# Kernel optimization log

Measured on AMD Instinct MI355X. Metric: run time of the kernel, lower is better.

Reference implementation:

```python
import jax, jax.numpy as jnp
import numpy as np

B, T, D, H, KH, HD, F, L, V = 2, 2048, 1024, 16, 4, 64, 4096, 4, 32000
G = H // KH  # num_key_value_groups
EPS = 1e-6
SCALE = HD ** -0.5


def setup_inputs() -> dict:
    key = jax.random.key(0)
    ks = jax.random.split(key, 8)
    std = 0.02
    return {
        "input_ids": jax.random.randint(ks[0], (B, T), 0, V, dtype=jnp.int32),
        "embed_w": jax.random.normal(ks[1], (V, D), jnp.float32) * std,
        "pos_w": jax.random.normal(ks[2], (T, D), jnp.float32) * std,
        "ln1_w": jnp.ones((L, D), jnp.float32),
        "ln2_w": jnp.ones((L, D), jnp.float32),
        "wq": jax.random.normal(ks[3], (L, D, H * HD), jnp.float32) * std,
        "wkv": jax.random.normal(ks[4], (L, D, 2 * KH * HD), jnp.float32) * std,
        "wo": jax.random.normal(ks[5], (L, H * HD, D), jnp.float32) * std,
        "w1": jax.random.normal(ks[6], (L, D, F), jnp.float32) * std,
        "w2": jax.random.normal(ks[7], (L, F, D), jnp.float32) * std,
        "norm_w": jnp.ones((D,), jnp.float32),
    }


def _rmsnorm(x, w):
    return x * jax.lax.rsqrt(jnp.mean(x * x, axis=-1, keepdims=True) + EPS) * w


def reference(input_ids, embed_w, pos_w, ln1_w, ln2_w, wq, wkv, wo, w1, w2, norm_w):
    causal = jnp.tril(jnp.ones((T, T), dtype=bool))  # True = keep
    x = embed_w[input_ids] + pos_w[:T]  # [B,T,D]
    for l in range(L):
        h = _rmsnorm(x, ln1_w[l])
        q = (h @ wq[l]).reshape(B, T, H, HD)
        kv = h @ wkv[l]
        k, v = jnp.split(kv, 2, axis=-1)
        k = jnp.repeat(k.reshape(B, T, KH, HD), G, axis=2)  # GQA repeat_interleave
        v = jnp.repeat(v.reshape(B, T, KH, HD), G, axis=2)
        scores = jnp.einsum("bqhd,bkhd->bhqk", q, k) * SCALE
        scores = jnp.where(causal, scores, -jnp.inf)
        p = jax.nn.softmax(scores, axis=-1)
        o = jnp.einsum("bhqk,bkhd->bqhd", p, v).reshape(B, T, H * HD)
        x = x + o @ wo[l]
        h = _rmsnorm(x, ln2_w[l])
        x = x + jax.nn.gelu(h @ w1[l], approximate=False) @ w2[l]
    x = _rmsnorm(x, norm_w)
    logits = x @ embed_w.T  # tied lm_head
    return logits
```

## Files before the change

### kernel.cpp

```cpp
#include <hip/hip_runtime.h>
#include <hip/hip_bf16.h>

#define DI __device__ __forceinline__

typedef unsigned short u16;
typedef unsigned int u32;
typedef __attribute__((ext_vector_type(8))) short bf16x8;
typedef __attribute__((ext_vector_type(4))) short bf16x4;
typedef __attribute__((ext_vector_type(4))) float f32x4;

#define B_   2
#define T_   2048
#define D_   1024
#define H_   16
#define KH_  4
#define HD_  64
#define F_   4096
#define L_   4
#define V_   32000
#define M_   (B_ * T_)
#define QKVN (H_*HD_ + 2*KH_*HD_)

DI u16 f2bf(float f) {
  __hip_bfloat16 h = __float2bfloat16(f);
  return *reinterpret_cast<u16*>(&h);
}

DI float bf2f(u16 b) {
  __hip_bfloat16 h = *reinterpret_cast<__hip_bfloat16*>(&b);
  return __bfloat162float(h);
}

DI void gl_lds16(const void* g, void* l) {
  __builtin_amdgcn_global_load_lds(
      (const __attribute__((address_space(1))) u32*)g,
      (__attribute__((address_space(3))) u32*)l, 16, 0, 0);
}

#define BARRIER() do { asm volatile("" ::: "memory"); __builtin_amdgcn_s_barrier(); asm volatile("" ::: "memory"); } while (0)
#define LGK0()    asm volatile("s_waitcnt lgkmcnt(0)" ::: "memory")
#define VMC(n)    asm volatile("s_waitcnt vmcnt(" #n ")" ::: "memory")
#define PRIO(p)   __builtin_amdgcn_s_setprio(p)

__global__ __launch_bounds__(256) void embed_kernel(const int* __restrict__ ids,
                                                    const float* __restrict__ ew,
                                                    const float* __restrict__ pw,
                                                    float* __restrict__ x) {
  const int row = blockIdx.x;
  const int t = row & (T_ - 1);
  const int id = ids[row];
  float4 e = reinterpret_cast<const float4*>(ew + (size_t)id * D_)[threadIdx.x];
  float4 p = reinterpret_cast<const float4*>(pw + (size_t)t * D_)[threadIdx.x];
  e.x += p.x; e.y += p.y; e.z += p.z; e.w += p.w;
  reinterpret_cast<float4*>(x + (size_t)row * D_)[threadIdx.x] = e;
}

__global__ __launch_bounds__(256) void conv_kernel(const float* __restrict__ W,
                                                   u16* __restrict__ Wb) {
  const size_t i = (size_t)blockIdx.x * 256 + threadIdx.x;
  float4 v = reinterpret_cast<const float4*>(W)[i];
  ushort4 ov;
  ov.x = f2bf(v.x); ov.y = f2bf(v.y); ov.z = f2bf(v.z); ov.w = f2bf(v.w);
  reinterpret_cast<ushort4*>(Wb)[i] = ov;
}

__global__ __launch_bounds__(256) void convt_fused(const float* __restrict__ wq,
                                                   const float* __restrict__ wkv,
                                                   const float* __restrict__ wo,
                                                   const float* __restrict__ w1,
                                                   const float* __restrict__ w2,
                                                   u16* __restrict__ wtq,
                                                   u16* __restrict__ wto,
                                                   u16* __restrict__ wt1,
                                                   u16* __restrict__ wt2) {
  const int t = blockIdx.x;
  const float* W; u16* Wt; int K, N, local;
  if (t < 1024)      { W = wq;  Wt = wtq;               K = 1024; N = 1024; local = t; }
  else if (t < 1536) { W = wkv; Wt = wtq + 1024*1024;   K = 1024; N = 512;  local = t - 1024; }
  else if (t < 2560) { W = wo;  Wt = wto;               K = 1024; N = 1024; local = t - 1536; }
  else if (t < 6656) { W = w1;  Wt = wt1;               K = 1024; N = 4096; local = t - 2560; }
  else               { W = w2;  Wt = wt2;               K = 4096; N = 1024; local = t - 6656; }
  const int nk = K >> 5;
  const int k0 = (local % nk) * 32, n0 = (local / nk) * 32;
  __shared__ float tb[32][33];
  const int tx = threadIdx.x & 31, ty = threadIdx.x >> 5;
  #pragma unroll
  for (int i = 0; i < 4; i++)
    tb[ty + i*8][tx] = W[(size_t)(k0 + ty + i*8) * N + n0 + tx];
  __syncthreads();
  #pragma unroll
  for (int i = 0; i < 4; i++)
    Wt[(size_t)(n0 + ty + i*8) * K + k0 + tx] = f2bf(tb[tx][ty + i*8]);
}

__global__ __launch_bounds__(256) void rmsnorm_kernel(const float* __restrict__ x,
                                                      const float* __restrict__ w,
                                                      u16* __restrict__ out) {
  const int row = blockIdx.x;
  const int tid = threadIdx.x;
  float4 v = reinterpret_cast<const float4*>(x + (size_t)row * D_)[tid];
  float ss = v.x*v.x + v.y*v.y + v.z*v.z + v.w*v.w;
  #pragma unroll
  for (int off = 32; off > 0; off >>= 1) ss += __shfl_down(ss, off, 64);
  __shared__ float red[4];
  if ((tid & 63) == 0) red[tid >> 6] = ss;
  __syncthreads();
  const float tot = red[0] + red[1] + red[2] + red[3];
  const float rstd = rsqrtf(tot * (1.0f / D_) + 1e-6f);
  float4 wv = reinterpret_cast<const float4*>(w)[tid];
  ushort4 ov;
  ov.x = f2bf(v.x * rstd * wv.x);
  ov.y = f2bf(v.y * rstd * wv.y);
  ov.z = f2bf(v.z * rstd * wv.z);
  ov.w = f2bf(v.w * rstd * wv.w);
  reinterpret_cast<ushort4*>(out + (size_t)row * D_)[tid] = ov;
}

template <int EPI>
__global__ __launch_bounds__(256) void gemm_bt(const u16* __restrict__ A,
                                               const u16* __restrict__ Bt,
                                               const float* __restrict__ res,
                                               u16* __restrict__ Cb,
                                               float* __restrict__ Cf,
                                               int M, int N, int K) {
  __shared__ u16 As[128 * 64];
  __shared__ u16 Bs[128 * 64];
  const int tid = threadIdx.x;
  const int n0 = blockIdx.x * 128;
  const int m0 = blockIdx.y * 128;
  const int lane = tid & 63, wave = tid >> 6;
  const int wm = wave >> 1, wn = wave & 1;
  const int l15 = lane & 15, l4 = lane >> 4;
  const int srow = tid >> 3, scol = (tid & 7) * 8;
  const u16* ag = A + (size_t)(m0 + srow) * K + scol;
  const u16* bg = Bt + (size_t)(n0 + srow) * K + scol;
  u16* asd = &As[srow * 64 + scol];
  u16* bsd = &Bs[srow * 64 + scol];
  f32x4 acc[4][4] = {};
  const int nk = K >> 6;
  for (int kt = 0; kt < nk; kt++) {
    const int k0 = kt * 64;
    __syncthreads();
    #pragma unroll
    for (int i = 0; i < 4; i++) gl_lds16(ag + (size_t)i*32*K + k0, asd + i*32*64);
    #pragma unroll
    for (int i = 0; i < 4; i++) gl_lds16(bg + (size_t)i*32*K + k0, bsd + i*32*64);
    __syncthreads();
    #pragma unroll
    for (int s = 0; s < 2; s++) {
      bf16x8 af[4], bfv[4];
      #pragma unroll
      for (int i = 0; i < 4; i++)
        af[i] = *reinterpret_cast<const bf16x8*>(&As[(wm*64 + i*16 + l15)*64 + s*32 + l4*8]);
      #pragma unroll
      for (int j = 0; j < 4; j++)
        bfv[j] = *reinterpret_cast<const bf16x8*>(&Bs[(wn*64 + j*16 + l15)*64 + s*32 + l4*8]);
      #pragma unroll
      for (int i = 0; i < 4; i++)
        #pragma unroll
        for (int j = 0; j < 4; j++)
          acc[i][j] = __builtin_amdgcn_mfma_f32_16x16x32_bf16(bfv[j], af[i], acc[i][j], 0, 0, 0);
    }
  }
  #pragma unroll
  for (int i = 0; i < 4; i++) {
    const int row = m0 + wm*64 + i*16 + l15;
    #pragma unroll
    for (int j = 0; j < 4; j++) {
      const int colb = n0 + wn*64 + j*16 + l4*4;
      const size_t idx = (size_t)row * N + colb;
      const f32x4 v = acc[i][j];
      if (EPI == 0) {
        ushort4 ov;
        ov.x = f2bf(v[0]); ov.y = f2bf(v[1]); ov.z = f2bf(v[2]); ov.w = f2bf(v[3]);
        *reinterpret_cast<ushort4*>(&Cb[idx]) = ov;
      } else {
        const float4 rv = *reinterpret_cast<const float4*>(&res[idx]);
        float4 ov;
        ov.x = v[0] + rv.x; ov.y = v[1] + rv.y; ov.z = v[2] + rv.z; ov.w = v[3] + rv.w;
        *reinterpret_cast<float4*>(&Cf[idx]) = ov;
      }
    }
  }
}

template <int EPI>
__global__ __launch_bounds__(512, 2) void gemm256(const u16* __restrict__ A,
                                                  const u16* __restrict__ Bt,
                                                  u16* __restrict__ Cb,
                                                  float* __restrict__ Cf,
                                                  int M, int N, int K) {
  __shared__ char lds[131072];
  char* const AsB = lds;
  char* const BsB = lds + 65536;
  const int tid = threadIdx.x;
  const int lane = tid & 63, wave = tid >> 6;
  const int wm = wave >> 2, wn = wave & 3;
  const int l15 = lane & 15, l4 = lane >> 4;

  const int nm = M >> 8;
  const int nwg = nm * (N >> 8);
  const int cpx = nwg >> 3;
  const int bid = blockIdx.x;
  const int wg = (bid & 7) * cpx + (bid >> 3);
  const int m0 = (wg % nm) << 8;
  const int n0 = (wg / nm) << 8;

  const u16* const Atile = A + (size_t)m0 * K;
  const u16* const Btile = Bt + (size_t)n0 * K;

  int soff[2][2], pd[2][2];
  #pragma unroll
  for (int h = 0; h < 2; ++h)
    #pragma unroll
    for (int jj = 0; jj < 2; ++jj) {
      const int row = h*128 + jj*64 + (tid >> 3);
      const int sl  = (tid & 7) ^ (row & 7);
      soff[h][jj] = row * K + sl * 8;
      pd[h][jj]   = h*16384 + jj*8192 + tid*16;
    }
  const int swz = (l15 & 7) << 4;
  const int rb0 = l15*128 + ((l4*16)      ^ swz);
  const int rb1 = l15*128 + ((64 + l4*16) ^ swz);

  #define STA(S,H,T) do { const u16* g_ = Atile + (T)*64; char* d_ = AsB + (S)*32768; \
      gl_lds16(g_ + soff[H][0], d_ + pd[H][0]); gl_lds16(g_ + soff[H][1], d_ + pd[H][1]); } while (0)
  #define STB(S,H,T) do { const u16* g_ = Btile + (T)*64; char* d_ = BsB + (S)*32768; \
      gl_lds16(g_ + soff[H][0], d_ + pd[H][0]); gl_lds16(g_ + soff[H][1], d_ + pd[H][1]); } while (0)
  #define RDA(S,GI,RB) (*reinterpret_cast<const bf16x8*>(AsB + (S)*32768 + (GI)*2048 + (RB)))
  #define RDB(S,GJ,RB) (*reinterpret_cast<const bf16x8*>(BsB + (S)*32768 + (GJ)*2048 + (RB)))

  f32x4 acc[8][4] = {};
  bf16x8 Ar[4][2], Br[4][2];

  #define RDA03(S) { _Pragma("unroll") for (int i=0;i<4;++i){ Ar[i][0]=RDA(S,i*2+wm,rb0); Ar[i][1]=RDA(S,i*2+wm,rb1);} }
  #define RDA47(S) { _Pragma("unroll") for (int i=0;i<4;++i){ Ar[i][0]=RDA(S,(i+4)*2+wm,rb0); Ar[i][1]=RDA(S,(i+4)*2+wm,rb1);} }
  #define RDB01(S) { _Pragma("unroll") for (int j=0;j<2;++j){ Br[j][0]=RDB(S,j*4+wn,rb0); Br[j][1]=RDB(S,j*4+wn,rb1);} }
  #define RDB23(S) { _Pragma("unroll") for (int j=2;j<4;++j){ Br[j][0]=RDB(S,j*4+wn,rb0); Br[j][1]=RDB(S,j*4+wn,rb1);} }
  #define MFQ(IO,JL) { _Pragma("unroll") for (int i=0;i<4;++i) _Pragma("unroll") for (int jj=0;jj<2;++jj) { \
      acc[(IO)+i][(JL)+jj] = __builtin_amdgcn_mfma_f32_16x16x32_bf16(Br[(JL)+jj][0], Ar[i][0], acc[(IO)+i][(JL)+jj],0,0,0); \
      acc[(IO)+i][(JL)+jj] = __builtin_amdgcn_mfma_f32_16x16x32_bf16(Br[(JL)+jj][1], Ar[i][1], acc[(IO)+i][(JL)+jj],0,0,0); } }

  STA(0,0,0); STA(0,1,0); STB(0,0,0); STB(0,1,0);
  VMC(4);
  STA(1,0,1); STB(1,0,1); STB(1,1,1);
  VMC(6);
  BARRIER();

  const int niter = K >> 7;
  for (int it = 0; it < niter; ++it) {
    const int t0 = it*2, t1 = t0 + 1;
    const bool pf = (it + 1 < niter);
    RDA03(0); RDB01(0); STA(1,1,t1);
    BARRIER(); LGK0(); PRIO(1); MFQ(0,0); PRIO(0); BARRIER();
    RDB23(0); if (pf) STA(0,0,t0+2);
    BARRIER(); LGK0(); PRIO(1); MFQ(0,2); PRIO(0); BARRIER();
    RDA47(0); if (pf) STB(0,0,t0+2);
    BARRIER(); LGK0(); PRIO(1); MFQ(4,0); PRIO(0); BARRIER();
    if (pf) { STB(0,1,t0+2); VMC(6); } else { VMC(0); }
    BARRIER(); PRIO(1); MFQ(4,2); PRIO(0); BARRIER();
    RDA03(1); RDB01(1); if (pf) STA(0,1,t0+2);
    BARRIER(); LGK0(); PRIO(1); MFQ(0,0); PRIO(0); BARRIER();
    RDB23(1); if (pf) STA(1,0,t1+2);
    BARRIER(); LGK0(); PRIO(1); MFQ(0,2); PRIO(0); BARRIER();
    RDA47(1); if (pf) STB(1,0,t1+2);
    BARRIER(); LGK0(); PRIO(1); MFQ(4,0); PRIO(0); BARRIER();
    if (pf) { STB(1,1,t1+2); VMC(6); }
    BARRIER(); PRIO(1); MFQ(4,2); PRIO(0); BARRIER();
  }

  #pragma unroll
  for (int i = 0; i < 8; ++i) {
    const int row = m0 + (i*2 + wm)*16 + l15;
    #pragma unroll
    for (int j = 0; j < 4; ++j) {
      const int colb = n0 + (j*4 + wn)*16 + l4*4;
      const f32x4 v = acc[i][j];
      if (EPI == 0) {
        *reinterpret_cast<f32x4*>(&Cf[(size_t)row * N + colb]) = v;
      } else {
        ushort4 ov;
        #pragma unroll
        for (int rr = 0; rr < 4; ++rr) {
          const float g = 0.5f * v[rr] * (1.0f + erff(v[rr] * 0.70710678118f));
          ((u16*)&ov)[rr] = f2bf(g);
        }
        *reinterpret_cast<ushort4*>(&Cb[(size_t)row * N + colb]) = ov;
      }
    }
  }
  #undef STA
  #undef STB
  #undef RDA
  #undef RDB
  #undef RDA03
  #undef RDA47
  #undef RDB01
  #undef RDB23
  #undef MFQ
}

__global__ __launch_bounds__(512) void attn_kernel(const u16* __restrict__ qkv,
                                                   u16* __restrict__ o) {
  const int qt = blockIdx.x;
  const int h  = blockIdx.y;
  const int b  = blockIdx.z;
  const int kh = h / (H_ / KH_);
  __shared__ u16 Ks[2][64 * 64];
  __shared__ u16 Vt[64 * 66];
  __shared__ u16 Pl[8][16 * 68];
  const int tid = threadIdx.x, lane = tid & 63, wave = tid >> 6;
  const int l15 = lane & 15, l4 = lane >> 4;
  const size_t Mrow = (size_t)b * T_;

  bf16x8 qf[2];
  {
    const u16* qp = qkv + (Mrow + qt*128 + wave*16 + l15) * QKVN + h*HD_ + l4*8;
    qf[0] = *reinterpret_cast<const bf16x8*>(qp);
    qf[1] = *reinterpret_cast<const bf16x8*>(qp + 32);
    #pragma unroll
    for (int s = 0; s < 2; s++)
      #pragma unroll
      for (int j = 0; j < 8; j++)
        qf[s][j] = (short)f2bf(bf2f((u16)qf[s][j]) * 0.18033688f);
  }
  float m_run = -1e30f, l_run = 0.0f;
  f32x4 oacc[4] = {};

  const int srow = tid >> 3, scol = (tid & 7) * 8;
  const int vp = (tid >> 4) * 2;
  const int vd = (tid & 15) * 4;
  const u16* const kbase = qkv + Mrow * QKVN + D_ + kh*HD_;
  const u16* const vbase = kbase + KH_*HD_;

  {
    gl_lds16(kbase + (size_t)srow * QKVN + scol, &Ks[0][srow*64 + scol]);
    const u16* vg = vbase + (size_t)vp * QKVN + vd;
    bf16x4 v0 = *reinterpret_cast<const bf16x4*>(vg);
    bf16x4 v1 = *reinterpret_cast<const bf16x4*>(vg + QKVN);
    #pragma unroll
    for (int j = 0; j < 4; j++) {
      const u32 pk = (u32)(u16)v0[j] | ((u32)(u16)v1[j] << 16);
      *reinterpret_cast<u32*>(&Vt[(vd + j)*66 + vp]) = pk;
    }
  }
  __syncthreads();

  const int nkt = 2*qt + 2;
  for (int kt = 0; kt < nkt; kt++) {
    const int cur = kt & 1;
    const bool pf = kt + 1 < nkt;
    bf16x4 v0n, v1n;
    if (pf) {
      gl_lds16(kbase + (size_t)((kt+1)*64 + srow) * QKVN + scol,
               &Ks[1-cur][srow*64 + scol]);
      const u16* vg = vbase + (size_t)((kt+1)*64 + vp) * QKVN + vd;
      v0n = *reinterpret_cast<const bf16x4*>(vg);
      v1n = *reinterpret_cast<const bf16x4*>(vg + QKVN);
    }

    f32x4 sa[4] = {};
    #pragma unroll
    for (int s = 0; s < 2; s++)
      #pragma unroll
      for (int n = 0; n < 4; n++) {
        bf16x8 kf = *reinterpret_cast<const bf16x8*>(&Ks[cur][(n*16 + l15)*64 + s*32 + l4*8]);
        sa[n] = __builtin_amdgcn_mfma_f32_16x16x32_bf16(kf, qf[s], sa[n], 0, 0, 0);
      }
    if (kt >= 2*qt) {
      const int qloc = wave*16 + l15;
      const int kbase_loc = kt*64 - qt*128 + l4*4;
      #pragma unroll
      for (int n = 0; n < 4; n++) {
        #pragma unroll
        for (int r = 0; r < 4; r++)
          if (kbase_loc + n*16 + r > qloc) sa[n][r] = -1e30f;
      }
    }
    float mx;
    {
      f32x4 m4;
      #pragma unroll
      for (int r = 0; r < 4; r++)
        m4[r] = fmaxf(fmaxf(sa[0][r], sa[1][r]), fmaxf(sa[2][r], sa[3][r]));
      mx = fmaxf(fmaxf(m4[0], m4[1]), fmaxf(m4[2], m4[3]));
      mx = fmaxf(mx, __shfl_xor(mx, 16, 64));
      mx = fmaxf(mx, __shfl_xor(mx, 32, 64));
    }
    if (__any((int)(mx - m_run > 8.0f))) {
      const float nm = fmaxf(m_run, mx);
      const float alpha = exp2f(m_run - nm);
      m_run = nm;
      l_run *= alpha;
      #pragma unroll
      for (int r = 0; r < 4; r++) {
        const float a_r = __shfl(alpha, l4*4 + r, 64);
        #pragma unroll
        for (int n = 0; n < 4; n++) oacc[n][r] *= a_r;
      }
    }
    float rs = 0.0f;
    u16* pw = &Pl[wave][0];
    #pragma unroll
    for (int n = 0; n < 4; n++) {
      ushort4 pv;
      #pragma unroll
      for (int r = 0; r < 4; r++) {
        const float p = exp2f(sa[n][r] - m_run);
        rs += p;
        ((u16*)&pv)[r] = f2bf(p);
      }
      *reinterpret_cast<ushort4*>(&pw[l15*68 + n*16 + l4*4]) = pv;
    }
    rs += __shfl_xor(rs, 16, 64);
    rs += __shfl_xor(rs, 32, 64);
    l_run += rs;

    asm volatile("s_waitcnt lgkmcnt(0)" ::: "memory");
    #pragma unroll
    for (int s = 0; s < 2; s++) {
      bf16x8 pa = *reinterpret_cast<const bf16x8*>(&Pl[wave][l15*68 + s*32 + l4*8]);
      #pragma unroll
      for (int n = 0; n < 4; n++) {
        bf16x8 vb = *reinterpret_cast<const bf16x8*>(&Vt[(n*16 + l15)*66 + s*32 + l4*8]);
        oacc[n] = __builtin_amdgcn_mfma_f32_16x16x32_bf16(pa, vb, oacc[n], 0, 0, 0);
      }
    }
    __syncthreads();
    if (pf) {
      #pragma unroll
      for (int j = 0; j < 4; j++) {
        const u32 pk = (u32)(u16)v0n[j] | ((u32)(u16)v1n[j] << 16);
        *reinterpret_cast<u32*>(&Vt[(vd + j)*66 + vp]) = pk;
      }
      __syncthreads();
    }
  }
  float lr[4];
  #pragma unroll
  for (int r = 0; r < 4; r++) lr[r] = __shfl(l_run, l4*4 + r, 64);
  #pragma unroll
  for (int n = 0; n < 4; n++)
    #pragma unroll
    for (int r = 0; r < 4; r++) {
      const float ov = oacc[n][r] / lr[r];
      const size_t row = Mrow + qt*128 + wave*16 + l4*4 + r;
      o[row * (size_t)(H_*HD_) + h*HD_ + n*16 + l15] = f2bf(ov);
    }
}

#define OFF_X     0ull
#define OFF_H     16777216ull
#define OFF_QKV   25165824ull
#define OFF_O     37748736ull
#define OFF_U     46137344ull
#define OFF_WTQ   79691776ull
#define OFF_WTO   82837504ull
#define OFF_WT1   84934656ull
#define OFF_WT2   93323264ull
#define OFF_EBF   101711872ull

extern "C" void kernel_launch(void* const* d_in, const int* in_sizes, int n_in,
                              void* d_out, int out_size, void* d_ws, size_t ws_size,
                              hipStream_t stream) {
  const int*   ids = (const int*)  d_in[0];
  const float* ew  = (const float*)d_in[1];
  const float* pw  = (const float*)d_in[2];
  const float* ln1 = (const float*)d_in[3];
  const float* ln2 = (const float*)d_in[4];
  const float* wq  = (const float*)d_in[5];
  const float* wkv = (const float*)d_in[6];
  const float* wo  = (const float*)d_in[7];
  const float* w1  = (const float*)d_in[8];
  const float* w2  = (const float*)d_in[9];
  const float* nw  = (const float*)d_in[10];
  float* out = (float*)d_out;

  char* ws = (char*)d_ws;
  float* x   = (float*)(ws + OFF_X);
  u16*   h   = (u16*)  (ws + OFF_H);
  u16*   qkv = (u16*)  (ws + OFF_QKV);
  u16*   o   = (u16*)  (ws + OFF_O);
  u16*   u   = (u16*)  (ws + OFF_U);
  u16*   wtq = (u16*)  (ws + OFF_WTQ);
  u16*   wto = (u16*)  (ws + OFF_WTO);
  u16*   wt1 = (u16*)  (ws + OFF_WT1);
  u16*   wt2 = (u16*)  (ws + OFF_WT2);
  u16*   ebf = (u16*)  (ws + OFF_EBF);

  embed_kernel<<<M_, 256, 0, stream>>>(ids, ew, pw, x);
  conv_kernel<<<(V_*D_/4)/256, 256, 0, stream>>>(ew, ebf);

  for (int l = 0; l < L_; l++) {
    convt_fused<<<10752, 256, 0, stream>>>(
        wq  + (size_t)l*D_*(H_*HD_),
        wkv + (size_t)l*D_*(2*KH_*HD_),
        wo  + (size_t)l*(H_*HD_)*D_,
        w1  + (size_t)l*D_*F_,
        w2  + (size_t)l*F_*D_,
        wtq, wto, wt1, wt2);

    rmsnorm_kernel<<<M_, 256, 0, stream>>>(x, ln1 + (size_t)l*D_, h);
    gemm_bt<0><<<dim3(QKVN/128, M_/128), 256, 0, stream>>>(h, wtq, nullptr, qkv, nullptr, M_, QKVN, D_);
    attn_kernel<<<dim3(T_/128, H_, B_), 512, 0, stream>>>(qkv, o);
    gemm_bt<1><<<dim3(D_/128, M_/128), 256, 0, stream>>>(o, wto, x, nullptr, x, M_, D_, H_*HD_);
    rmsnorm_kernel<<<M_, 256, 0, stream>>>(x, ln2 + (size_t)l*D_, h);
    gemm256<1><<<dim3((F_/256)*(M_/256)), 512, 0, stream>>>(h, wt1, u, nullptr, M_, F_, D_);
    gemm_bt<1><<<dim3(D_/128, M_/128), 256, 0, stream>>>(u, wt2, x, nullptr, x, M_, D_, F_);
  }

  rmsnorm_kernel<<<M_, 256, 0, stream>>>(x, nw, h);
  gemm256<0><<<dim3((V_/256)*(M_/256)), 512, 0, stream>>>(h, ebf, nullptr, out, M_, V_, D_);
}
```

Before: 1.625 ms.

## Pair mirrored causal query tiles per attention block to balance work

Each attention block now handles two query tiles, qt and 15-qt, so every block does the same total number of causal key tiles. The two tiles share each staged K/V tile in LDS, cutting K/V loads. The grid is halved to 8x16x2 = 256 blocks, and the block carries two sets of accumulators and a doubled P buffer, which raises register and LDS pressure and may lower occupancy.

```diff
diff --git a/kernel.cpp b/kernel.cpp
--- a/kernel.cpp
+++ b/kernel.cpp
@@ -302,30 +302,36 @@
 
 __global__ __launch_bounds__(512) void attn_kernel(const u16* __restrict__ qkv,
                                                    u16* __restrict__ o) {
-  const int qt = blockIdx.x;
+  const int qtA = blockIdx.x;
+  const int qtB = 15 - qtA;
   const int h  = blockIdx.y;
   const int b  = blockIdx.z;
   const int kh = h / (H_ / KH_);
   __shared__ u16 Ks[2][64 * 64];
   __shared__ u16 Vt[64 * 66];
-  __shared__ u16 Pl[8][16 * 68];
+  __shared__ u16 Pl[16][16 * 68];
   const int tid = threadIdx.x, lane = tid & 63, wave = tid >> 6;
   const int l15 = lane & 15, l4 = lane >> 4;
   const size_t Mrow = (size_t)b * T_;
 
-  bf16x8 qf[2];
+  bf16x8 qfA[2], qfB[2];
   {
-    const u16* qp = qkv + (Mrow + qt*128 + wave*16 + l15) * QKVN + h*HD_ + l4*8;
-    qf[0] = *reinterpret_cast<const bf16x8*>(qp);
-    qf[1] = *reinterpret_cast<const bf16x8*>(qp + 32);
+    const u16* qpA = qkv + (Mrow + qtA*128 + wave*16 + l15) * QKVN + h*HD_ + l4*8;
+    const u16* qpB = qkv + (Mrow + qtB*128 + wave*16 + l15) * QKVN + h*HD_ + l4*8;
+    qfA[0] = *reinterpret_cast<const bf16x8*>(qpA);
+    qfA[1] = *reinterpret_cast<const bf16x8*>(qpA + 32);
+    qfB[0] = *reinterpret_cast<const bf16x8*>(qpB);
+    qfB[1] = *reinterpret_cast<const bf16x8*>(qpB + 32);
     #pragma unroll
     for (int s = 0; s < 2; s++)
       #pragma unroll
-      for (int j = 0; j < 8; j++)
-        qf[s][j] = (short)f2bf(bf2f((u16)qf[s][j]) * 0.18033688f);
-  }
-  float m_run = -1e30f, l_run = 0.0f;
-  f32x4 oacc[4] = {};
+      for (int j = 0; j < 8; j++) {
+        qfA[s][j] = (short)f2bf(bf2f((u16)qfA[s][j]) * 0.18033688f);
+        qfB[s][j] = (short)f2bf(bf2f((u16)qfB[s][j]) * 0.18033688f);
+      }
+  }
+  float mA = -1e30f, lA = 0.0f, mB = -1e30f, lB = 0.0f;
+  f32x4 oaccA[4] = {}, oaccB[4] = {};
 
   const int srow = tid >> 3, scol = (tid & 7) * 8;
   const int vp = (tid >> 4) * 2;
@@ -346,10 +352,11 @@
   }
   __syncthreads();
 
-  const int nkt = 2*qt + 2;
-  for (int kt = 0; kt < nkt; kt++) {
+  const int nktA = 2*qtA + 2;
+  const int nktB = 2*qtB + 2;
+  for (int kt = 0; kt < nktB; kt++) {
     const int cur = kt & 1;
-    const bool pf = kt + 1 < nkt;
+    const bool pf = kt + 1 < nktB;
     bf16x4 v0n, v1n;
     if (pf) {
       gl_lds16(kbase + (size_t)((kt+1)*64 + srow) * QKVN + scol,
@@ -359,73 +366,140 @@
       v1n = *reinterpret_cast<const bf16x4*>(vg + QKVN);
     }
 
-    f32x4 sa[4] = {};
-    #pragma unroll
-    for (int s = 0; s < 2; s++)
+    {
+      f32x4 sa[4] = {};
+      #pragma unroll
+      for (int s = 0; s < 2; s++)
+        #pragma unroll
+        for (int n = 0; n < 4; n++) {
+          bf16x8 kf = *reinterpret_cast<const bf16x8*>(&Ks[cur][(n*16 + l15)*64 + s*32 + l4*8]);
+          sa[n] = __builtin_amdgcn_mfma_f32_16x16x32_bf16(kf, qfB[s], sa[n], 0, 0, 0);
+        }
+      if (kt >= 2*qtB) {
+        const int qloc = wave*16 + l15;
+        const int kb = kt*64 - qtB*128 + l4*4;
+        #pragma unroll
+        for (int n = 0; n < 4; n++)
+          #pragma unroll
+          for (int r = 0; r < 4; r++)
+            if (kb + n*16 + r > qloc) sa[n][r] = -1e30f;
+      }
+      float mx;
+      {
+        f32x4 m4;
+        #pragma unroll
+        for (int r = 0; r < 4; r++)
+          m4[r] = fmaxf(fmaxf(sa[0][r], sa[1][r]), fmaxf(sa[2][r], sa[3][r]));
+        mx = fmaxf(fmaxf(m4[0], m4[1]), fmaxf(m4[2], m4[3]));
+        mx = fmaxf(mx, __shfl_xor(mx, 16, 64));
+        mx = fmaxf(mx, __shfl_xor(mx, 32, 64));
+      }
+      if (__any((int)(mx - mB > 8.0f))) {
+        const float nm = fmaxf(mB, mx);
+        const float alpha = exp2f(mB - nm);
+        mB = nm; lB *= alpha;
+        #pragma unroll
+        for (int r = 0; r < 4; r++) {
+          const float a_r = __shfl(alpha, l4*4 + r, 64);
+          #pragma unroll
+          for (int n = 0; n < 4; n++) oaccB[n][r] *= a_r;
+        }
+      }
+      float rs = 0.0f;
+      u16* pw = &Pl[8 + wave][0];
       #pragma unroll
       for (int n = 0; n < 4; n++) {
-        bf16x8 kf = *reinterpret_cast<const bf16x8*>(&Ks[cur][(n*16 + l15)*64 + s*32 + l4*8]);
-        sa[n] = __builtin_amdgcn_mfma_f32_16x16x32_bf16(kf, qf[s], sa[n], 0, 0, 0);
-      }
-    if (kt >= 2*qt) {
-      const int qloc = wave*16 + l15;
-      const int kbase_loc = kt*64 - qt*128 + l4*4;
+        ushort4 pv;
+        #pragma unroll
+        for (int r = 0; r < 4; r++) {
+          const float p = exp2f(sa[n][r] - mB);
+          rs += p;
+          ((u16*)&pv)[r] = f2bf(p);
+        }
+        *reinterpret_cast<ushort4*>(&pw[l15*68 + n*16 + l4*4]) = pv;
+      }
+      rs += __shfl_xor(rs, 16, 64);
+      rs += __shfl_xor(rs, 32, 64);
+      lB += rs;
+      asm volatile("s_waitcnt lgkmcnt(0)" ::: "memory");
+      #pragma unroll
+      for (int s = 0; s < 2; s++) {
+        bf16x8 pa = *reinterpret_cast<const bf16x8*>(&pw[l15*68 + s*32 + l4*8]);
+        #pragma unroll
+        for (int n = 0; n < 4; n++) {
+          bf16x8 vb = *reinterpret_cast<const bf16x8*>(&Vt[(n*16 + l15)*66 + s*32 + l4*8]);
+          oaccB[n] = __builtin_amdgcn_mfma_f32_16x16x32_bf16(pa, vb, oaccB[n], 0, 0, 0);
+        }
+      }
+    }
+
+    if (kt < nktA) {
+      f32x4 sa[4] = {};
+      #pragma unroll
+      for (int s = 0; s < 2; s++)
+        #pragma unroll
+        for (int n = 0; n < 4; n++) {
+          bf16x8 kf = *reinterpret_cast<const bf16x8*>(&Ks[cur][(n*16 + l15)*64 + s*32 + l4*8]);
+          sa[n] = __builtin_amdgcn_mfma_f32_16x16x32_bf16(kf, qfA[s], sa[n], 0, 0, 0);
+        }
+      if (kt >= 2*qtA) {
+        const int qloc = wave*16 + l15;
+        const int kb = kt*64 - qtA*128 + l4*4;
+        #pragma unroll
+        for (int n = 0; n < 4; n++)
+          #pragma unroll
+          for (int r = 0; r < 4; r++)
+            if (kb + n*16 + r > qloc) sa[n][r] = -1e30f;
+      }
+      float mx;
+      {
+        f32x4 m4;
+        #pragma unroll
+        for (int r = 0; r < 4; r++)
+          m4[r] = fmaxf(fmaxf(sa[0][r], sa[1][r]), fmaxf(sa[2][r], sa[3][r]));
+        mx = fmaxf(fmaxf(m4[0], m4[1]), fmaxf(m4[2], m4[3]));
+        mx = fmaxf(mx, __shfl_xor(mx, 16, 64));
+        mx = fmaxf(mx, __shfl_xor(mx, 32, 64));
+      }
+      if (__any((int)(mx - mA > 8.0f))) {
+        const float nm = fmaxf(mA, mx);
+        const float alpha = exp2f(mA - nm);
+        mA = nm; lA *= alpha;
+        #pragma unroll
+        for (int r = 0; r < 4; r++) {
+          const float a_r = __shfl(alpha, l4*4 + r, 64);
+          #pragma unroll
+          for (int n = 0; n < 4; n++) oaccA[n][r] *= a_r;
+        }
+      }
+      float rs = 0.0f;
+      u16* pw = &Pl[wave][0];
       #pragma unroll
       for (int n = 0; n < 4; n++) {
-        #pragma unroll
-        for (int r = 0; r < 4; r++)
-          if (kbase_loc + n*16 + r > qloc) sa[n][r] = -1e30f;
-      }
-    }
-    float mx;
-    {
-      f32x4 m4;
-      #pragma unroll
-      for (int r = 0; r < 4; r++)
-        m4[r] = fmaxf(fmaxf(sa[0][r], sa[1][r]), fmaxf(sa[2][r], sa[3][r]));
-      mx = fmaxf(fmaxf(m4[0], m4[1]), fmaxf(m4[2], m4[3]));
-      mx = fmaxf(mx, __shfl_xor(mx, 16, 64));
-      mx = fmaxf(mx, __shfl_xor(mx, 32, 64));
-    }
-    if (__any((int)(mx - m_run > 8.0f))) {
-      const float nm = fmaxf(m_run, mx);
-      const float alpha = exp2f(m_run - nm);
-      m_run = nm;
-      l_run *= alpha;
-      #pragma unroll
-      for (int r = 0; r < 4; r++) {
-        const float a_r = __shfl(alpha, l4*4 + r, 64);
-        #pragma unroll
-        for (int n = 0; n < 4; n++) oacc[n][r] *= a_r;
-      }
-    }
-    float rs = 0.0f;
-    u16* pw = &Pl[wave][0];
-    #pragma unroll
-    for (int n = 0; n < 4; n++) {
-      ushort4 pv;
-      #pragma unroll
-      for (int r = 0; r < 4; r++) {
-        const float p = exp2f(sa[n][r] - m_run);
-        rs += p;
-        ((u16*)&pv)[r] = f2bf(p);
-      }
-      *reinterpret_cast<ushort4*>(&pw[l15*68 + n*16 + l4*4]) = pv;
-    }
-    rs += __shfl_xor(rs, 16, 64);
-    rs += __shfl_xor(rs, 32, 64);
-    l_run += rs;
-
-    asm volatile("s_waitcnt lgkmcnt(0)" ::: "memory");
-    #pragma unroll
-    for (int s = 0; s < 2; s++) {
-      bf16x8 pa = *reinterpret_cast<const bf16x8*>(&Pl[wave][l15*68 + s*32 + l4*8]);
-      #pragma unroll
-      for (int n = 0; n < 4; n++) {
-        bf16x8 vb = *reinterpret_cast<const bf16x8*>(&Vt[(n*16 + l15)*66 + s*32 + l4*8]);
-        oacc[n] = __builtin_amdgcn_mfma_f32_16x16x32_bf16(pa, vb, oacc[n], 0, 0, 0);
-      }
-    }
+        ushort4 pv;
+        #pragma unroll
+        for (int r = 0; r < 4; r++) {
+          const float p = exp2f(sa[n][r] - mA);
+          rs += p;
+          ((u16*)&pv)[r] = f2bf(p);
+        }
+        *reinterpret_cast<ushort4*>(&pw[l15*68 + n*16 + l4*4]) = pv;
+      }
+      rs += __shfl_xor(rs, 16, 64);
+      rs += __shfl_xor(rs, 32, 64);
+      lA += rs;
+      asm volatile("s_waitcnt lgkmcnt(0)" ::: "memory");
+      #pragma unroll
+      for (int s = 0; s < 2; s++) {
+        bf16x8 pa = *reinterpret_cast<const bf16x8*>(&pw[l15*68 + s*32 + l4*8]);
+        #pragma unroll
+        for (int n = 0; n < 4; n++) {
+          bf16x8 vb = *reinterpret_cast<const bf16x8*>(&Vt[(n*16 + l15)*66 + s*32 + l4*8]);
+          oaccA[n] = __builtin_amdgcn_mfma_f32_16x16x32_bf16(pa, vb, oaccA[n], 0, 0, 0);
+        }
+      }
+    }
+
     __syncthreads();
     if (pf) {
       #pragma unroll
@@ -436,17 +510,29 @@
       __syncthreads();
     }
   }
-  float lr[4];
-  #pragma unroll
-  for (int r = 0; r < 4; r++) lr[r] = __shfl(l_run, l4*4 + r, 64);
-  #pragma unroll
-  for (int n = 0; n < 4; n++)
-    #pragma unroll
-    for (int r = 0; r < 4; r++) {
-      const float ov = oacc[n][r] / lr[r];
-      const size_t row = Mrow + qt*128 + wave*16 + l4*4 + r;
-      o[row * (size_t)(H_*HD_) + h*HD_ + n*16 + l15] = f2bf(ov);
-    }
+  {
+    float lr[4];
+    #pragma unroll
+    for (int r = 0; r < 4; r++) lr[r] = __shfl(lA, l4*4 + r, 64);
+    #pragma unroll
+    for (int n = 0; n < 4; n++)
+      #pragma unroll
+      for (int r = 0; r < 4; r++) {
+        const float ov = oaccA[n][r] / lr[r];
+        const size_t row = Mrow + qtA*128 + wave*16 + l4*4 + r;
+        o[row * (size_t)(H_*HD_) + h*HD_ + n*16 + l15] = f2bf(ov);
+      }
+    #pragma unroll
+    for (int r = 0; r < 4; r++) lr[r] = __shfl(lB, l4*4 + r, 64);
+    #pragma unroll
+    for (int n = 0; n < 4; n++)
+      #pragma unroll
+      for (int r = 0; r < 4; r++) {
+        const float ov = oaccB[n][r] / lr[r];
+        const size_t row = Mrow + qtB*128 + wave*16 + l4*4 + r;
+        o[row * (size_t)(H_*HD_) + h*HD_ + n*16 + l15] = f2bf(ov);
+      }
+  }
 }
 
 #define OFF_X     0ull
@@ -502,7 +588,7 @@
 
     rmsnorm_kernel<<<M_, 256, 0, stream>>>(x, ln1 + (size_t)l*D_, h);
     gemm_bt<0><<<dim3(QKVN/128, M_/128), 256, 0, stream>>>(h, wtq, nullptr, qkv, nullptr, M_, QKVN, D_);
-    attn_kernel<<<dim3(T_/128, H_, B_), 512, 0, stream>>>(qkv, o);
+    attn_kernel<<<dim3(T_/256, H_, B_), 512, 0, stream>>>(qkv, o);
     gemm_bt<1><<<dim3(D_/128, M_/128), 256, 0, stream>>>(o, wto, x, nullptr, x, M_, D_, H_*HD_);
     rmsnorm_kernel<<<M_, 256, 0, stream>>>(x, ln2 + (size_t)l*D_, h);
     gemm256<1><<<dim3((F_/256)*(M_/256)), 512, 0, stream>>>(h, wt1, u, nullptr, M_, F_, D_);
```

Result: no change. 1.598 ms (-1.7%).
